# Performance work log

Measured on AMD Instinct MI355X. Metric: run time of the kernel, lower is better.

The kernel has to match this reference:

```python
import jax, jax.numpy as jnp
import numpy as np

EPS = 1e-08


def setup_inputs() -> dict:
    key = jax.random.key(0)
    k1, k2 = jax.random.split(key)
    z = jax.random.normal(k1, (64, 768, 32, 32), dtype=jnp.float32)
    memory = jax.random.normal(k2, (100, 768), dtype=jnp.float32)
    return {"z": z, "memory": memory}


def _l2norm(x, axis=-1):
    # matches F.normalize(dim=-1): x / max(||x||, 1e-12)
    n = jnp.sqrt(jnp.sum(x * x, axis=axis, keepdims=True))
    return x / jnp.maximum(n, 1e-12)


def reference(z, memory):
    B, C, H, W = z.shape
    M = memory.shape[0]
    # (B,C,H,W) -> (B, N, C) with N = H*W
    z_flat = jnp.transpose(z, (0, 2, 3, 1)).reshape(B, H * W, C)
    z_norm = _l2norm(z_flat)
    mem_norm = _l2norm(memory)
    scores = jnp.einsum('bnc,mc->bnm', z_norm, mem_norm)  # (B, N, M)
    w = jax.nn.softmax(scores, axis=-1)
    lam = 1.0 / M
    d = w - lam
    attn_w = jax.nn.relu(d) * w / (jnp.abs(d) + EPS)      # hard shrinkage
    attn_w = attn_w / (jnp.sum(attn_w, axis=-1, keepdims=True) + EPS)
    z_hat_flat = jnp.einsum('bnm,mc->bnc', attn_w, memory)
    z_hat = jnp.transpose(z_hat_flat.reshape(B, H, W, C), (0, 3, 1, 2))
    return (z_hat, attn_w)
```

## Files before the change

kernel.cpp:

```cpp
#include <hip/hip_runtime.h>

#define EPSF 1e-8f

typedef __fp16   h2v   __attribute__((ext_vector_type(2)));
typedef _Float16 half8 __attribute__((ext_vector_type(8)));
typedef float    f32x16 __attribute__((ext_vector_type(16)));

constexpr int Bn = 64, Cc = 768, Nn = 1024, Mm = 100;

__device__ inline f32x16 zero16() {
    f32x16 z;
#pragma unroll
    for (int i = 0; i < 16; ++i) z[i] = 0.f;
    return z;
}

union U4H8 { uint4 u; half8 h; h2v p[4]; };

__device__ inline unsigned pkr(float a, float b) {
    union { h2v p; unsigned u; } cv;
    cv.p = __builtin_amdgcn_cvt_pkrtz(a, b);
    return cv.u;
}

__device__ inline void gload_lds16(const void* g, void* s) {
    __builtin_amdgcn_global_load_lds(
        (const __attribute__((address_space(1))) unsigned int*)g,
        (__attribute__((address_space(3))) unsigned int*)s, 16, 0, 0);
}

__global__ __launch_bounds__(256) void prep_kernel(const float* __restrict__ mem,
                                                   _Float16* __restrict__ mhiF,
                                                   _Float16* __restrict__ mloF,
                                                   _Float16* __restrict__ muF) {
    int m = blockIdx.x, t = threadIdx.x;
    float inv = 0.f;
    if (m < Mm) {
        float ss = 0.f;
        for (int c = t; c < Cc; c += 256) { float v = mem[m * Cc + c]; ss += v * v; }
        __shared__ float red[256];
        red[t] = ss; __syncthreads();
        for (int s = 128; s > 0; s >>= 1) { if (t < s) red[t] += red[t + s]; __syncthreads(); }
        inv = 1.f / fmaxf(sqrtf(red[0]), 1e-12f);
    }
    for (int c = t; c < Cc; c += 256) {
        float v = (m < Mm) ? mem[m * Cc + c] : 0.f;
        float nv = v * inv;
        _Float16 hh = (_Float16)nv;
        _Float16 ll = (_Float16)(nv - (float)hh);
        int cs = c >> 4, hb = (c >> 3) & 1, j = c & 7, mt = m >> 5, ml = m & 31;
        size_t idx = ((size_t)(cs * 4 + mt) * 64 + hb * 32 + ml) * 8 + j;
        mhiF[idx] = hh;
        mloF[idx] = ll;
        int ct = c >> 5, cl = c & 31, ms = m >> 4, hm = (m >> 3) & 1, jm = m & 7;
        size_t idx2 = ((size_t)(ct * 8 + ms) * 64 + hm * 32 + cl) * 8 + jm;
        muF[idx2] = (_Float16)v;
    }
}

__global__ __launch_bounds__(256) void score_kernel(
    const float* __restrict__ z, const _Float16* __restrict__ mhiF,
    const _Float16* __restrict__ mloF, float* __restrict__ attn_out) {
    __shared__ uint4 fbuf[2][4][2][256];

    const int tid = threadIdx.x;
    const int w = tid >> 6;
    const int l = tid & 63;
    const int wid = (blockIdx.x << 2) | w;
    const int b = wid >> 5;
    const int pxb = (wid & 31) * 32;
    const int pl = l & 31;
    const int h = l >> 5;
    const float* zr = z + (size_t)b * Cc * Nn + pxb + pl + (size_t)h * 8 * Nn;
    const uint4* mh4 = (const uint4*)mhiF;
    const uint4* ml4 = (const uint4*)mloF;
    const uint4* gh = mh4 + w * 64 + l;
    const uint4* gl = ml4 + w * 64 + l;

    f32x16 acc[4] = {zero16(), zero16(), zero16(), zero16()};
    float ss = 0.f;
    float zbufA[4][8], zbufB[4][8];

#pragma unroll
    for (int i = 0; i < 4; ++i) {
        gload_lds16(gh + i * 256, &fbuf[0][i][0][w * 64]);
        gload_lds16(gl + i * 256, &fbuf[0][i][1][w * 64]);
    }
#pragma unroll
    for (int i = 0; i < 4; ++i)
#pragma unroll
        for (int j = 0; j < 8; ++j)
            zbufA[i][j] = __builtin_nontemporal_load(&zr[(size_t)(i * 16 + j) * Nn]);
    __builtin_amdgcn_sched_barrier(0);
    asm volatile("s_waitcnt vmcnt(32)" ::: "memory");
    __builtin_amdgcn_sched_barrier(0);
    __builtin_amdgcn_s_barrier();
    __builtin_amdgcn_sched_barrier(0);

    auto round_body = [&](int RR, float (&ZC)[4][8], float (&ZN)[4][8], int FB) {
        const bool more = (RR + 1 < 12);
        if (more) {
#pragma unroll
            for (int i = 0; i < 4; ++i) {
                gload_lds16(gh + ((RR + 1) * 4 + i) * 256, &fbuf[FB ^ 1][i][0][w * 64]);
                gload_lds16(gl + ((RR + 1) * 4 + i) * 256, &fbuf[FB ^ 1][i][1][w * 64]);
            }
#pragma unroll
            for (int i = 0; i < 4; ++i)
#pragma unroll
                for (int j = 0; j < 8; ++j)
                    ZN[i][j] = __builtin_nontemporal_load(
                        &zr[(size_t)(((RR + 1) * 4 + i) * 16 + j) * Nn]);
        }
#pragma unroll
        for (int i = 0; i < 4; ++i) {
            U4H8 zh, zl8;
#pragma unroll
            for (int t = 0; t < 4; ++t) {
                float u = ZC[i][2 * t], v = ZC[i][2 * t + 1];
                h2v p = __builtin_amdgcn_cvt_pkrtz(u, v);
                zh.p[t] = p;
                zl8.p[t] = __builtin_amdgcn_cvt_pkrtz(u - (float)p.x, v - (float)p.y);
                ss += u * u + v * v;
            }
            U4H8 ah, al;
#pragma unroll
            for (int mt = 0; mt < 4; ++mt) {
                ah.u = fbuf[FB][i][0][mt * 64 + l];
                al.u = fbuf[FB][i][1][mt * 64 + l];
                acc[mt] = __builtin_amdgcn_mfma_f32_32x32x16_f16(ah.h, zh.h, acc[mt], 0, 0, 0);
                acc[mt] = __builtin_amdgcn_mfma_f32_32x32x16_f16(al.h, zh.h, acc[mt], 0, 0, 0);
                acc[mt] = __builtin_amdgcn_mfma_f32_32x32x16_f16(ah.h, zl8.h, acc[mt], 0, 0, 0);
            }
        }
        if (more) {
            __builtin_amdgcn_sched_barrier(0);
            asm volatile("s_waitcnt vmcnt(32)" ::: "memory");
            __builtin_amdgcn_sched_barrier(0);
            __builtin_amdgcn_s_barrier();
            __builtin_amdgcn_sched_barrier(0);
        }
    };

#pragma unroll 1
    for (int rp = 0; rp < 6; ++rp) {
        round_body(2 * rp, zbufA, zbufB, 0);
        round_body(2 * rp + 1, zbufB, zbufA, 1);
    }

    ss += __shfl_xor(ss, 32);
    float invn = 1.f / fmaxf(sqrtf(ss), 1e-12f);

    float a_[64];
#pragma unroll
    for (int r = 0; r < 64; ++r) {
        int mt = r >> 4, rr = r & 15;
        float v = acc[mt][rr] * invn;
        if (r >= 52) v = -3.0e38f;
        else if (r >= 48) v = (h == 0) ? v : -3.0e38f;
        a_[r] = v;
    }
    float mx = -3.0e38f;
#pragma unroll
    for (int r = 0; r < 52; ++r) mx = fmaxf(mx, a_[r]);
    mx = fmaxf(mx, __shfl_xor(mx, 32));

    float sum = 0.f;
#pragma unroll
    for (int r = 0; r < 52; ++r) { float e = expf(a_[r] - mx); a_[r] = e; sum += e; }
    sum += __shfl_xor(sum, 32);
    float itot = 1.f / sum;

    float asum = 0.f;
#pragma unroll
    for (int r = 0; r < 52; ++r) {
        float w_ = a_[r] * itot;
        float d = w_ - 0.01f;
        float aa = (d > 0.f) ? (d * w_) / (d + EPSF) : 0.f;
        a_[r] = aa; asum += aa;
    }
    asum += __shfl_xor(asum, 32);
    float ia = 1.f / (asum + EPSF);
#pragma unroll
    for (int r = 0; r < 52; ++r) a_[r] *= ia;

    {
        size_t ob = (size_t)(wid * 32 + pl) * (size_t)Mm;
#pragma unroll
        for (int g = 0; g < 13; ++g) {
            int r0 = g * 4;
            int m0 = (r0 >> 4) * 32 + 8 * ((r0 >> 2) & 3) + 4 * h;
            if (g < 12 || h == 0) {
                float4 v = make_float4(a_[r0], a_[r0 + 1], a_[r0 + 2], a_[r0 + 3]);
                *(float4*)&attn_out[ob + m0] = v;
            }
        }
    }
}

__global__ __launch_bounds__(256, 4) void recon_kernel(
    const _Float16* __restrict__ muF, const float* __restrict__ attn_out,
    float* __restrict__ zhat) {
    const int tid = threadIdx.x;
    const int w = tid >> 6;
    const int l = tid & 63;
    const int orig = blockIdx.x;
    const int gb = (orig & 7) * 256 + (orig >> 3);
    const int b = gb >> 5;
    const int pxb = (gb & 31) * 32;
    const int pl = l & 31;
    const int h = l >> 5;

    const float* ap = attn_out + (size_t)(gb * 32 + pl) * (size_t)Mm;
    uint4 bfr[8];
#pragma unroll
    for (int ms = 0; ms < 6; ++ms) {
        float4 fa = *(const float4*)&ap[ms * 16 + h * 8];
        float4 fb = *(const float4*)&ap[ms * 16 + h * 8 + 4];
        bfr[ms] = make_uint4(pkr(fa.x, fa.y), pkr(fa.z, fa.w),
                             pkr(fb.x, fb.y), pkr(fb.z, fb.w));
    }
    {
        float4 fa = (h == 0) ? *(const float4*)&ap[96] : make_float4(0.f, 0.f, 0.f, 0.f);
        bfr[6] = make_uint4(pkr(fa.x, fa.y), pkr(fa.z, fa.w), 0u, 0u);
        bfr[7] = make_uint4(0u, 0u, 0u, 0u);
    }

    const uint4* mu4 = (const uint4*)muF;
    float* zo = zhat + (size_t)b * Cc * Nn + pxb + pl;
    const int ct0 = w * 6;
#pragma unroll 1
    for (int cti = 0; cti < 6; cti += 2) {
        int ct = ct0 + cti;
        f32x16 a2 = zero16(), a3 = zero16();
#pragma unroll
        for (int ms = 0; ms < 7; ++ms) {
            U4H8 A0, A1, Bf;
            A0.u = mu4[(ct * 8 + ms) * 64 + l];
            A1.u = mu4[((ct + 1) * 8 + ms) * 64 + l];
            Bf.u = bfr[ms];
            a2 = __builtin_amdgcn_mfma_f32_32x32x16_f16(A0.h, Bf.h, a2, 0, 0, 0);
            a3 = __builtin_amdgcn_mfma_f32_32x32x16_f16(A1.h, Bf.h, a3, 0, 0, 0);
        }
#pragma unroll
        for (int r = 0; r < 16; ++r) {
            int cl = (r & 3) + 8 * (r >> 2) + 4 * h;
            zo[(size_t)(ct * 32 + cl) * Nn] = a2[r];
            zo[(size_t)(ct * 32 + 32 + cl) * Nn] = a3[r];
        }
    }
}

extern "C" void kernel_launch(void* const* d_in, const int* in_sizes, int n_in,
                              void* d_out, int out_size, void* d_ws, size_t ws_size,
                              hipStream_t stream) {
    const float* z = (const float*)d_in[0];
    const float* mem = (const float*)d_in[1];
    float* out = (float*)d_out;
    float* zhat = out;
    float* attn = out + (size_t)Bn * Cc * Nn;
    _Float16* mhiF = (_Float16*)d_ws;
    _Float16* mloF = mhiF + 48 * 4 * 64 * 8;
    _Float16* muF = mloF + 48 * 4 * 64 * 8;

    prep_kernel<<<128, 256, 0, stream>>>(mem, mhiF, mloF, muF);
    score_kernel<<<512, 256, 0, stream>>>(z, mhiF, mloF, attn);
    recon_kernel<<<2048, 256, 0, stream>>>(muF, attn, zhat);
}
```

Measured before the change: 105.7 us.

## Fuse score and reconstruction kernels, feeding attention weights from registers

Merges the score/softmax kernel and the reconstruction kernel into a single kernel. The normalized attention weights are packed to fp16 straight from registers, with cross-half lane shuffles building the MFMA B operand, so attn no longer has to be re-read from global memory in a second kernel. Each wave now processes all 24 channel tiles for its 32 pixels, and block indices are swizzled across groups of 8. The trade-off is far less parallelism in the reconstruction phase (512 blocks doing 4x the work per wave instead of 2048 blocks), plus higher register pressure in one kernel.

After: 94.85 us. 1.11x faster.

```diff
diff --git a/kernel.cpp b/kernel.cpp
--- a/kernel.cpp
+++ b/kernel.cpp
@@ -58,15 +58,18 @@
     }
 }
 
-__global__ __launch_bounds__(256) void score_kernel(
+__global__ __launch_bounds__(256) void fused_kernel(
     const float* __restrict__ z, const _Float16* __restrict__ mhiF,
-    const _Float16* __restrict__ mloF, float* __restrict__ attn_out) {
+    const _Float16* __restrict__ mloF, const _Float16* __restrict__ muF,
+    float* __restrict__ zhat, float* __restrict__ attn_out) {
     __shared__ uint4 fbuf[2][4][2][256];
 
     const int tid = threadIdx.x;
     const int w = tid >> 6;
     const int l = tid & 63;
-    const int wid = (blockIdx.x << 2) | w;
+    const int orig = blockIdx.x;
+    const int gbblk = (orig & 7) * 64 + (orig >> 3);
+    const int wid = (gbblk << 2) | w;
     const int b = wid >> 5;
     const int pxb = (wid & 31) * 32;
     const int pl = l & 31;
@@ -183,6 +186,8 @@
     float ia = 1.f / (asum + EPSF);
 #pragma unroll
     for (int r = 0; r < 52; ++r) a_[r] *= ia;
+#pragma unroll
+    for (int r = 52; r < 64; ++r) a_[r] = 0.f;
 
     {
         size_t ob = (size_t)(wid * 32 + pl) * (size_t)Mm;
@@ -196,42 +201,30 @@
             }
         }
     }
-}
-
-__global__ __launch_bounds__(256, 4) void recon_kernel(
-    const _Float16* __restrict__ muF, const float* __restrict__ attn_out,
-    float* __restrict__ zhat) {
-    const int tid = threadIdx.x;
-    const int w = tid >> 6;
-    const int l = tid & 63;
-    const int orig = blockIdx.x;
-    const int gb = (orig & 7) * 256 + (orig >> 3);
-    const int b = gb >> 5;
-    const int pxb = (gb & 31) * 32;
-    const int pl = l & 31;
-    const int h = l >> 5;
-
-    const float* ap = attn_out + (size_t)(gb * 32 + pl) * (size_t)Mm;
+
     uint4 bfr[8];
 #pragma unroll
-    for (int ms = 0; ms < 6; ++ms) {
-        float4 fa = *(const float4*)&ap[ms * 16 + h * 8];
-        float4 fb = *(const float4*)&ap[ms * 16 + h * 8 + 4];
-        bfr[ms] = make_uint4(pkr(fa.x, fa.y), pkr(fa.z, fa.w),
-                             pkr(fb.x, fb.y), pkr(fb.z, fb.w));
-    }
-    {
-        float4 fa = (h == 0) ? *(const float4*)&ap[96] : make_float4(0.f, 0.f, 0.f, 0.f);
-        bfr[6] = make_uint4(pkr(fa.x, fa.y), pkr(fa.z, fa.w), 0u, 0u);
-        bfr[7] = make_uint4(0u, 0u, 0u, 0u);
+    for (int mt = 0; mt < 4; ++mt) {
+        unsigned p0 = pkr(a_[16 * mt + 0], a_[16 * mt + 1]);
+        unsigned p1 = pkr(a_[16 * mt + 2], a_[16 * mt + 3]);
+        unsigned p2 = pkr(a_[16 * mt + 4], a_[16 * mt + 5]);
+        unsigned p3 = pkr(a_[16 * mt + 6], a_[16 * mt + 7]);
+        unsigned p4 = pkr(a_[16 * mt + 8], a_[16 * mt + 9]);
+        unsigned p5 = pkr(a_[16 * mt + 10], a_[16 * mt + 11]);
+        unsigned p6 = pkr(a_[16 * mt + 12], a_[16 * mt + 13]);
+        unsigned p7 = pkr(a_[16 * mt + 14], a_[16 * mt + 15]);
+        unsigned s0 = __shfl_xor(p0, 32), s1 = __shfl_xor(p1, 32);
+        unsigned s2 = __shfl_xor(p2, 32), s3 = __shfl_xor(p3, 32);
+        unsigned s4 = __shfl_xor(p4, 32), s5 = __shfl_xor(p5, 32);
+        unsigned s6 = __shfl_xor(p6, 32), s7 = __shfl_xor(p7, 32);
+        bfr[2 * mt]     = h ? make_uint4(s2, s3, p2, p3) : make_uint4(p0, p1, s0, s1);
+        bfr[2 * mt + 1] = h ? make_uint4(s6, s7, p6, p7) : make_uint4(p4, p5, s4, s5);
     }
 
     const uint4* mu4 = (const uint4*)muF;
     float* zo = zhat + (size_t)b * Cc * Nn + pxb + pl;
-    const int ct0 = w * 6;
 #pragma unroll 1
-    for (int cti = 0; cti < 6; cti += 2) {
-        int ct = ct0 + cti;
+    for (int ct = 0; ct < 24; ct += 2) {
         f32x16 a2 = zero16(), a3 = zero16();
 #pragma unroll
         for (int ms = 0; ms < 7; ++ms) {
@@ -264,6 +257,5 @@
     _Float16* muF = mloF + 48 * 4 * 64 * 8;
 
     prep_kernel<<<128, 256, 0, stream>>>(mem, mhiF, mloF, muF);
-    score_kernel<<<512, 256, 0, stream>>>(z, mhiF, mloF, attn);
-    recon_kernel<<<2048, 256, 0, stream>>>(muF, attn, zhat);
-}
+    fused_kernel<<<512, 256, 0, stream>>>(z, mhiF, mloF, muF, zhat, attn);
+}
```
